# Optimization experiments

Hardware: AMD Instinct MI355X
Metric: run time of the kernel (lower is better)

The kernel has to match this reference:

```python
import jax, jax.numpy as jnp
import numpy as np

N, E = 2048, 262144
H, EH, NH, FF = 96, 64, 12, 192
DH = H // NH
NITERS, NLAYERS = 2, 3


def _leaky(x):
    return jax.nn.leaky_relu(x, 0.01)


def _ln(x, s, b):
    m = x.mean(-1, keepdims=True)
    v = ((x - m) ** 2).mean(-1, keepdims=True)
    return (x - m) / jnp.sqrt(v + 1e-5) * s + b


def _encoder(x, qkv_w, qkv_b, out_w, out_b, l1s, l1b, fw1, fb1, fw2, fb2, l2s, l2b):
    qkv = x @ qkv_w + qkv_b  # [N, 3H]
    q, k, v = jnp.split(qkv, 3, axis=-1)
    q = q.reshape(-1, NH, DH)
    k = k.reshape(-1, NH, DH)
    v = v.reshape(-1, NH, DH)
    att = jax.nn.softmax(jnp.einsum('nhd,mhd->hnm', q, k) / jnp.sqrt(jnp.float32(DH)), axis=-1)
    o = jnp.einsum('hnm,mhd->nhd', att, v).reshape(-1, H) @ out_w + out_b
    x = _ln(x + o, l1s, l1b)
    f = jax.nn.relu(x @ fw1 + fb1) @ fw2 + fb2
    return _ln(x + f, l2s, l2b)


def setup_inputs() -> dict:
    key = jax.random.key(0)
    ks = iter(jax.random.split(key, 64))
    def p(shape, scale=0.05):
        return (jax.random.normal(next(ks), shape) * scale).astype(jnp.float32)
    inp = {}
    inp['X'] = jax.random.normal(next(ks), (N, 19), dtype=jnp.float32)
    inp['edge_features'] = jax.random.uniform(next(ks), (E, 12), dtype=jnp.float32)
    inp['edge_index'] = jax.random.randint(next(ks), (E, 2), 0, N, dtype=jnp.int32)
    inp['node_scaler'] = jnp.ones((19,), jnp.float32)
    inp['edge_scaler'] = jnp.ones((12,), jnp.float32)
    inp['in_w1'] = p((19, H)); inp['in_b1'] = p((H,))
    inp['in_w2'] = p((H, H)); inp['in_b2'] = p((H,))
    inp['enc_qkv_w'] = p((NLAYERS, H, 3 * H)); inp['enc_qkv_b'] = p((NLAYERS, 3 * H))
    inp['enc_out_w'] = p((NLAYERS, H, H)); inp['enc_out_b'] = p((NLAYERS, H))
    inp['enc_ln1_s'] = jnp.ones((NLAYERS, H), jnp.float32); inp['enc_ln1_b'] = jnp.zeros((NLAYERS, H), jnp.float32)
    inp['enc_ff_w1'] = p((NLAYERS, H, FF)); inp['enc_ff_b1'] = p((NLAYERS, FF))
    inp['enc_ff_w2'] = p((NLAYERS, FF, H)); inp['enc_ff_b2'] = p((NLAYERS, H))
    inp['enc_ln2_s'] = jnp.ones((NLAYERS, H), jnp.float32); inp['enc_ln2_b'] = jnp.zeros((NLAYERS, H), jnp.float32)
    inp['ein_w1'] = p((12, EH)); inp['ein_b1'] = p((EH,))
    inp['ein_w2'] = p((EH, EH)); inp['ein_b2'] = p((EH,))
    inp['ad_w1'] = p((EH, EH)); inp['ad_b1'] = p((EH,))
    inp['ad_w2'] = p((EH, 1)); inp['ad_b2'] = p((1,))
    inp['ar_w1'] = p((EH, EH)); inp['ar_b1'] = p((EH,))
    inp['ar_w2'] = p((EH, 1)); inp['ar_b2'] = p((1,))
    inp['gc_w1'] = p((NITERS, 2 * H, 2 * H)); inp['gc_b1'] = p((NITERS, 2 * H))
    inp['gc_w2'] = p((NITERS, 2 * H, H)); inp['gc_b2'] = p((NITERS, H))
    inp['en_w1'] = p((2 * H + 12 + EH, H)); inp['en_b1'] = p((H,))
    inp['en_w2'] = p((H, 1)); inp['en_b2'] = p((1,))
    return inp


def reference(X, edge_features, edge_index, node_scaler, edge_scaler,
              in_w1, in_b1, in_w2, in_b2,
              enc_qkv_w, enc_qkv_b, enc_out_w, enc_out_b,
              enc_ln1_s, enc_ln1_b, enc_ff_w1, enc_ff_b1, enc_ff_w2, enc_ff_b2,
              enc_ln2_s, enc_ln2_b,
              ein_w1, ein_b1, ein_w2, ein_b2,
              ad_w1, ad_b1, ad_w2, ad_b2,
              ar_w1, ar_b1, ar_w2, ar_b2,
              gc_w1, gc_b1, gc_w2, gc_b2,
              en_w1, en_b1, en_w2, en_b2):
    ef = (edge_features + 1e-4) / edge_scaler
    x = X / node_scaler
    # edge feature MLP + direct/reverse attention weights
    ef_nn = _leaky(_leaky(ef @ ein_w1 + ein_b1) @ ein_w2 + ein_b2)
    a_dir = jax.nn.sigmoid(_leaky(ef_nn @ ad_w1 + ad_b1) @ ad_w2 + ad_b2)
    a_rev = jax.nn.sigmoid(_leaky(ef_nn @ ar_w1 + ar_b1) @ ar_w2 + ar_b2)
    alpha = jnp.concatenate([a_dir, a_rev], axis=0)  # [2E, 1]
    # node input MLP + transformer encoder over all N nodes
    h = _leaky(_leaky(x @ in_w1 + in_b1) @ in_w2 + in_b2)
    for i in range(NLAYERS):
        h = _encoder(h, enc_qkv_w[i], enc_qkv_b[i], enc_out_w[i], enc_out_b[i],
                     enc_ln1_s[i], enc_ln1_b[i], enc_ff_w1[i], enc_ff_b1[i],
                     enc_ff_w2[i], enc_ff_b2[i], enc_ln2_s[i], enc_ln2_b[i])
    src = edge_index[:, 0]
    dst = edge_index[:, 1]
    zeros_n = jnp.zeros((N,), edge_index.dtype)
    ind1 = jnp.concatenate([zeros_n, src, dst])  # destinations, [N + 2E]
    ind2 = jnp.concatenate([zeros_n, dst, src])  # sources
    alpha_full = jnp.concatenate([jnp.ones((N, 1), h.dtype), alpha], axis=0)
    for i in range(NITERS):
        m = jnp.concatenate([h[ind1], h[ind2]], axis=-1)  # [N+2E, 2H]
        m = _leaky(_leaky(m @ gc_w1[i] + gc_b1[i]) @ gc_w2[i] + gc_b2[i])
        num = jax.ops.segment_sum(alpha_full * m, ind1, num_segments=N)
        den = jax.ops.segment_sum(alpha_full, ind1, num_segments=N)
        h = num / (den + 1e-8)
    e = jnp.concatenate([h[src], h[dst], ef_nn, ef], axis=-1)
    pred = jax.nn.sigmoid(_leaky(e @ en_w1 + en_b1) @ en_w2 + en_b2)
    return pred
```

## Files before the change

kernel.cpp:

```cpp
#include <hip/hip_runtime.h>

#define NN 2048
#define EE 262144

typedef __attribute__((ext_vector_type(8))) short bf16x8;
typedef __attribute__((ext_vector_type(4))) float f32x4;
typedef unsigned int u32;
typedef unsigned short u16;

__device__ __forceinline__ u16 f2bf(float f){
  u32 u = __builtin_bit_cast(u32, f);
  u32 r = u + 0x7FFFu + ((u >> 16) & 1u);
  return (u16)(r >> 16);
}
__device__ __forceinline__ float bf2f(u16 h){
  u32 u = ((u32)h) << 16;
  return __builtin_bit_cast(float, u);
}
__device__ __forceinline__ int swzb(int byte, int row){ return byte ^ ((row & 7) << 4); }
__device__ __forceinline__ float lrelu(float v){ return v > 0.f ? v : 0.01f * v; }

static const size_t WS_WT    = 0;
static const size_t WS_EFNN  = 772096;
static const size_t WS_ALPHA = WS_EFNN  + 33554432;
static const size_t WS_H     = WS_ALPHA + 2097152;
static const size_t WS_QKV   = WS_H     + 786432;
static const size_t WS_OBUF  = WS_QKV   + 2359296;
static const size_t WS_TMPA  = WS_OBUF  + 786432;
static const size_t WS_TMPB  = WS_TMPA  + 786432;
static const size_t WS_X1    = WS_TMPB  + 1572864;
static const size_t WS_NUM   = WS_X1    + 786432;
static const size_t WS_DEN   = WS_NUM   + 786432;
static const size_t WS_XS    = WS_DEN   + 8192;
static const size_t WS_HBF   = WS_XS    + 155648;
static const size_t WS_SIDX  = WS_HBF   + 393216;
static const size_t WS_ALPS  = WS_SIDX  + 4194304;
static const size_t WS_CNT   = WS_ALPS  + 2097152;
static const size_t WS_OFFS  = WS_CNT   + 8192;
static const size_t WS_PK    = WS_OFFS  + 8192;

#define IN1T 0
#define IN2T 3072
#define QKVT 12288
#define OUTT 95232
#define FF1T 122880
#define FF2T 178176
#define EIN1T 233472
#define EIN2T 235520
#define AD1T 239616
#define AR1T 243712
#define GC1T 247808
#define GC2T 321536
#define ENAT 358400
#define ENBT 367616
#define ENCT 376832
#define POOL_TOT 386048

#define PK_EIN1 0
#define PK_EIN2 2048
#define PK_AD1  6144
#define PK_AR1  10240
#define PK_GC2  14336
#define PK_ENC  51200
#define PK_QKV  60416
#define PK_OUT  143360
#define PK_FF1  171008
#define PK_FF2  226304
#define PK_IN1  281600
#define PK_IN2  284672
#define PK_GC1A 293888
#define PK_GC1B 330752
#define PK_ENA  367616
#define PK_ENB  376832
#define PK_TOT  386048

struct CvtJobs {
  const float* src[27];
  int K[27], Nc[27], Kp[27];
  int cum[28];
};

__global__ __launch_bounds__(256) void k_cvt(CvtJobs jb, u16* __restrict__ pool){
  int i = blockIdx.x * 256 + threadIdx.x;
  if (i >= jb.cum[27]) return;
  int j = 0;
  while (i >= jb.cum[j + 1]) j++;
  int loc = i - jb.cum[j];
  int Kp = jb.Kp[j];
  int n = loc / Kp, k = loc - n * Kp;
  float v = (k < jb.K[j]) ? jb.src[j][(size_t)k * jb.Nc[j] + n] : 0.f;
  pool[i] = f2bf(v);
}

struct PkJobs {
  int srcOff[27], Nc16[27], Kp[27];
  int cum[28];
};

__global__ __launch_bounds__(256) void k_pack(PkJobs jb, const u16* __restrict__ pool,
                                              u16* __restrict__ pk){
  int i = blockIdx.x * 256 + threadIdx.x;
  if (i >= jb.cum[27]) return;
  int j = 0;
  while (i >= jb.cum[j + 1]) j++;
  int loc = i - jb.cum[j];
  int jj = loc & 7, lane = (loc >> 3) & 63, tk = loc >> 9;
// ... 48 lines not shown
  int pos = offs[i1] + r;
  sidx[pos] = make_int2(i1, i2);
  alphaS[pos] = alpha[g];
}

__global__ __launch_bounds__(256) void k_dens(const int* __restrict__ offs, const float* __restrict__ alphaS,
                                              float* __restrict__ den){
  int n = blockIdx.x * 4 + (threadIdx.x >> 6);
  int lane = threadIdx.x & 63;
  int b = offs[n], e = offs[n + 1];
  float s = 0.f;
  for (int i = b + lane; i < e; i += 64) s += alphaS[i];
  #pragma unroll
  for (int st = 1; st < 64; st <<= 1) s += __shfl_xor(s, st);
  if (lane == 0) den[n] = s + (n == 0 ? 2048.f : 0.f);
}

template<int NT, int KS, int SR, int NC16>
__device__ __forceinline__ void tile_gemm_gp(const char* sm, int aBase, const u16* __restrict__ Wp,
                                             int lane, f32x4* acc){
  const int r15 = lane & 15;
  const int kb = (lane >> 4) * 16;
  #pragma unroll
  for (int ks = 0; ks < KS; ks++){
    bf16x8 a = *(const bf16x8*)(sm + aBase + swzb(r15*SR + ks*64 + kb, r15));
    #pragma unroll
    for (int ct = 0; ct < NT; ct++){
      bf16x8 b = *(const bf16x8*)(Wp + (((size_t)ks*NC16 + ct)*64 + lane)*8);
      acc[ct] = __builtin_amdgcn_mfma_f32_16x16x32_bf16(a, b, acc[ct], 0, 0, 0);
    }
  }
}

template<int NT, int KS, int MODE, int ACT>
__global__ __launch_bounds__(256) void k_gemm2(const float* __restrict__ A, int K, int NcTot, int Nc16Tot,
    const u16* __restrict__ pkW, const float* __restrict__ bias, float* __restrict__ C,
    float* __restrict__ C2, const float* __restrict__ R, const float* __restrict__ sc,
    const float* __restrict__ bi)
{
  constexpr int Kpad = KS * 32;
  constexpr int SR = (Kpad*2 + 127) / 128 * 128;
  __shared__ __align__(16) char smem[32*SR + 256];
  const int tid = threadIdx.x;
  const int row0 = blockIdx.x * 32;
  for (int j = tid; j < 32*(Kpad/2); j += 256){
    int r = j / (Kpad/2); int c = (j - r*(Kpad/2)) * 2;
    const float* ap = A + (size_t)(row0 + r)*K + c;
    float f0 = (c < K) ? ap[0] : 0.f;
    float f1 = (c + 1 < K) ? ap[1] : 0.f;
    *(u32*)(smem + swzb(r*SR + c*2, r)) = (u32)f2bf(f0) | ((u32)f2bf(f1) << 16);
  }
  __syncthreads();
  const int lane = tid & 63, w = tid >> 6;
  const int wr = w >> 1, wc = w & 1;
  const int r15 = lane & 15;
  const int kb = (lane >> 4) * 16;
  f32x4 acc[NT] = {};
  #pragma unroll
  for (int ks = 0; ks < KS; ks++){
    int row = wr*16 + r15;
    bf16x8 a = *(const bf16x8*)(smem + swzb(row*SR + ks*64 + kb, row));
    #pragma unroll
    for (int ct = 0; ct < NT; ct++){
      int t16g = blockIdx.y*(2*NT) + wc*NT + ct;
      bf16x8 b = *(const bf16x8*)(pkW + (((size_t)ks*Nc16Tot + t16g)*64 + lane)*8);
      acc[ct] = __builtin_amdgcn_mfma_f32_16x16x32_bf16(a, b, acc[ct], 0, 0, 0);
    }
  }
  const int colbase = blockIdx.y*(NT*32) + wc*(NT*16);
  if (MODE != 2){
    #pragma unroll
    for (int ct = 0; ct < NT; ct++){
      int col = colbase + ct*16 + r15;
      float bs = bias ? bias[col] : 0.f;
      #pragma unroll
      for (int q = 0; q < 4; q++){
        int row = row0 + wr*16 + (lane >> 4)*4 + q;
        float v = acc[ct][q] + bs;
        if (ACT == 1) v = lrelu(v);
        if (ACT == 2) v = v > 0.f ? v : 0.f;
        if (MODE == 0){
          C[(size_t)row*NcTot + col] = v;
// ... 186 lines not shown
  for (int j = tid; j < 2048; j += 256){
    int r = j >> 5;
    ((u32*)efnn)[e0*32 + j] = *(const u32*)(smem + swzb(r*128 + (j&31)*4, r));
  }
  { f32x4 acc[4] = {};
    tile_gemm_gp<4,2,128,4>(smem, w*2048, pk + PK_AD1, lane, acc);
    store_lds(acc, 8192, adb1); }
  __syncthreads();
  { int row = tid >> 2, part = tid & 3;
    float s = 0.f;
    #pragma unroll
    for (int i = 0; i < 16; i++){
      int k = part*16 + i;
      s += bf2f(*(const u16*)(smem + 8192 + swzb(row*128 + k*2, row))) * adw2[k];
    }
    s += __shfl_xor(s, 1); s += __shfl_xor(s, 2);
    if (part == 0) alpha[e0 + row] = 1.f / (1.f + __expf(-(s + adb2[0]))); }
  __syncthreads();
  { f32x4 acc[4] = {};
    tile_gemm_gp<4,2,128,4>(smem, w*2048, pk + PK_AR1, lane, acc);
    store_lds(acc, 8192, arb1); }
  __syncthreads();
  { int row = tid >> 2, part = tid & 3;
    float s = 0.f;
    #pragma unroll
    for (int i = 0; i < 16; i++){
      int k = part*16 + i;
      s += bf2f(*(const u16*)(smem + 8192 + swzb(row*128 + k*2, row))) * arw2[k];
    }
    s += __shfl_xor(s, 1); s += __shfl_xor(s, 2);
    if (part == 0) alpha[EE + e0 + row] = 1.f / (1.f + __expf(-(s + arb2[0]))); }
}

__global__ __launch_bounds__(256) void k_gc5x(const float* __restrict__ P1, const float* __restrict__ P2,
    const int2* __restrict__ sidx, const float* __restrict__ alphaS, const int* __restrict__ offs,
    const u16* __restrict__ wt2p, const float* __restrict__ b2, const float* __restrict__ den,
    float* __restrict__ hout)
{
  __shared__ __align__(16) char smem[26624];
  float* p1c  = (float*)(smem + 24576);
  int*   i2b  = (int*)  (smem + 25344);
  float* alph = (float*)(smem + 25600);
  float* part = (float*)(smem + 25856);
  const int tid = threadIdx.x;
  const int lane = tid & 63, w = tid >> 6;
  const int wr = w >> 1, wc = w & 1;
  const int r15 = lane & 15;
  const int kb = (lane >> 4) * 16;
  const int n = blockIdx.x;
  const int rbeg = offs[n], rend = offs[n + 1];
  if (tid < 48) ((float4*)p1c)[tid] = ((const float4*)(P1 + (size_t)n*192))[tid];
  bf16x8 Bf[6][3];
  #pragma unroll
  for (int ks = 0; ks < 6; ks++)
    #pragma unroll
    for (int ct = 0; ct < 3; ct++)
      Bf[ks][ct] = *(const bf16x8*)(wt2p + (((size_t)ks*6 + wc*3 + ct)*64 + lane)*8);
  float b2r[3];
  #pragma unroll
  for (int ct = 0; ct < 3; ct++) b2r[ct] = b2[wc*48 + ct*16 + r15];
  float cs0 = 0.f, cs1 = 0.f, cs2 = 0.f;

  const int total = rend - rbeg + (n == 0 ? 1 : 0);
  const int nch = (total + 63) >> 6;
  for (int c = 0; c < nch; c++){
    int base = rbeg + c*64;
    if (tid < 64){
      int pos = base + tid;
      if (pos < rend){ i2b[tid] = sidx[pos].y; alph[tid] = alphaS[pos]; }
      else if (n == 0 && pos == rend){ i2b[tid] = 0; alph[tid] = 2048.f; }
      else { i2b[tid] = 0; alph[tid] = 0.f; }
    }
    __syncthreads();
    for (int j = tid; j < 1536; j += 256){
      int r = j / 24, q = j - (j/24)*24;
      int c8 = q * 8;
      const float* p2 = P2 + (size_t)i2b[r]*192 + c8;
      float4 b0 = *(const float4*)p2, b1 = *(const float4*)(p2 + 4);
      const float* pc = p1c + c8;
      u16 pkv[8];
      pkv[0]=f2bf(lrelu(pc[0]+b0.x)); pkv[1]=f2bf(lrelu(pc[1]+b0.y));
      pkv[2]=f2bf(lrelu(pc[2]+b0.z)); pkv[3]=f2bf(lrelu(pc[3]+b0.w));
      pkv[4]=f2bf(lrelu(pc[4]+b1.x)); pkv[5]=f2bf(lrelu(pc[5]+b1.y));
      pkv[6]=f2bf(lrelu(pc[6]+b1.z)); pkv[7]=f2bf(lrelu(pc[7]+b1.w));
      *(bf16x8*)(smem + swzb(r*384 + c8*2, r)) = *(bf16x8*)pkv;
    }
    __syncthreads();
    float ar[2][4];
    #pragma unroll
    for (int rt = 0; rt < 2; rt++)
      #pragma unroll
      for (int q = 0; q < 4; q++)
        ar[rt][q] = alph[wr*32 + rt*16 + (lane >> 4)*4 + q];
    f32x4 acc2[2][3] = {};
    #pragma unroll
    for (int ks = 0; ks < 6; ks++){
      bf16x8 a[2];
      #pragma unroll
      for (int rt = 0; rt < 2; rt++){
        int row = wr*32 + rt*16 + r15;
        a[rt] = *(const bf16x8*)(smem + swzb(row*384 + ks*64 + kb, row));
      }
      #pragma unroll
      for (int ct = 0; ct < 3; ct++)
        #pragma unroll
        for (int rt = 0; rt < 2; rt++)
          acc2[rt][ct] = __builtin_amdgcn_mfma_f32_16x16x32_bf16(a[rt], Bf[ks][ct], acc2[rt][ct], 0, 0, 0);
    }
    #pragma unroll
    for (int rt = 0; rt < 2; rt++){
      #pragma unroll
      for (int q = 0; q < 4; q++){
        float aw = ar[rt][q];
        cs0 += aw * lrelu(acc2[rt][0][q] + b2r[0]);
        cs1 += aw * lrelu(acc2[rt][1][q] + b2r[1]);
        cs2 += aw * lrelu(acc2[rt][2][q] + b2r[2]);
      }
    }
    __syncthreads();
  }
  #pragma unroll
  for (int stx = 16; stx < 64; stx <<= 1){
    cs0 += __shfl_xor(cs0, stx);
    cs1 += __shfl_xor(cs1, stx);
    cs2 += __shfl_xor(cs2, stx);
  }
  if (lane < 16){
    part[(w*3 + 0)*16 + lane] = cs0;
    part[(w*3 + 1)*16 + lane] = cs1;
    part[(w*3 + 2)*16 + lane] = cs2;
  }
  __syncthreads();
  if (tid < 96){
    int wc2 = tid / 48, rem = tid - wc2*48;
    int ct = rem / 16, rr = rem - ct*16;
    float tot = part[(wc2*3 + ct)*16 + rr] + part[((2 + wc2)*3 + ct)*16 + rr];
    hout[(size_t)n*96 + tid] = tot / (den[n] + 1e-8f);
  }
}

__global__ __launch_bounds__(256) void k_final2(const float* __restrict__ hp1, const float* __restrict__ hp2,
    const int* __restrict__ ei, const u16* __restrict__ efnn, const float* __restrict__ efr,
    const float* __restrict__ es, const u16* __restrict__ encp,
    const float* __restrict__ enw2, const float* __restrict__ enb2, float* __restrict__ out)
{
  __shared__ __align__(16) char smem[38144];
  float* etb = (float*)(smem + 12288);
  float* w2s = (float*)(smem + 37120);
  int*   eix = (int*)  (smem + 37504);
  const int tid = threadIdx.x;
  const int e0 = blockIdx.x * 64;
  for (int j = tid; j < 768; j += 256){
    int r = j / 12, q = j - (j/12)*12;
    int e = e0 + r;
    bf16x8 v;
    if (q < 8){
      v = *(const bf16x8*)(efnn + (size_t)e*64 + q*8);
    } else if (q < 10){
      u16 pkv[8];
      #pragma unroll
      for (int i = 0; i < 8; i++){
        int cc = (q - 8)*8 + i;
        pkv[i] = (cc < 12) ? f2bf((efr[(size_t)e*12 + cc] + 1e-4f) / es[cc]) : (u16)0;
      }
      v = *(bf16x8*)pkv;
    } else {
      v = bf16x8{0,0,0,0,0,0,0,0};
    }
    *(bf16x8*)(smem + swzb(r*192 + q*16, r)) = v;
  }
  if (tid < 96) w2s[tid] = enw2[tid];
  if (tid < 64){ eix[2*tid] = ei[2*(e0+tid)]; eix[2*tid+1] = ei[2*(e0+tid)+1]; }
  __syncthreads();
  const int lane = tid & 63, w = tid >> 6;
  const int r15 = lane & 15;
  f32x4 acc[6] = {};
  tile_gemm_gp<6,3,192,6>(smem, w*16*192, encp, lane, acc);
  #pragma unroll
  for (int ct = 0; ct < 6; ct++){
    int col = ct*16 + r15;
    #pragma unroll
    for (int q = 0; q < 4; q++){
      int row = w*16 + (lane >> 4)*4 + q;
      etb[row*97 + col] = acc[ct][q];
    }
  }
  __syncthreads();
  int r = tid >> 2, part = tid & 3;
  int s1 = eix[2*r], s2 = eix[2*r + 1];
  const float* p1 = hp1 + (size_t)s1*96 + part*24;
  const float* p2 = hp2 + (size_t)s2*96 + part*24;
  const float* et = etb + r*97 + part*24;
  const float* wz = w2s + part*24;
  float s = 0.f;
  #pragma unroll
  for (int i = 0; i < 24; i++){
    float v = et[i] + p1[i] + p2[i];
    s += lrelu(v) * wz[i];
  }
  s += __shfl_xor(s, 1); s += __shfl_xor(s, 2);
  if (part == 0) out[e0 + r] = 1.f / (1.f + __expf(-(s + enb2[0])));
}

extern "C" void kernel_launch(void* const* d_in, const int* in_sizes, int n_in,
                              void* d_out, int out_size, void* d_ws, size_t ws_size,
                              hipStream_t stream) {
  (void)in_sizes; (void)n_in; (void)out_size; (void)ws_size;
  const float* X      = (const float*)d_in[0];
  const float* EFR    = (const float*)d_in[1];
  const int*   EI     = (const int*)  d_in[2];
  const float* NS     = (const float*)d_in[3];
  const float* ES     = (const float*)d_in[4];
  const float* IN_W1  = (const float*)d_in[5];
  const float* IN_B1  = (const float*)d_in[6];
  const float* IN_W2  = (const float*)d_in[7];
  const float* IN_B2  = (const float*)d_in[8];
  const float* QKV_W  = (const float*)d_in[9];
  const float* QKV_B  = (const float*)d_in[10];
  const float* OUT_W  = (const float*)d_in[11];
  const float* OUT_B  = (const float*)d_in[12];
  const float* LN1S   = (const float*)d_in[13];
  const float* LN1B   = (const float*)d_in[14];
  const float* FFW1   = (const float*)d_in[15];
  const float* FFB1   = (const float*)d_in[16];
  const float* FFW2   = (const float*)d_in[17];
  const float* FFB2   = (const float*)d_in[18];
  const float* LN2S   = (const float*)d_in[19];
  const float* LN2B   = (const float*)d_in[20];
  const float* EIN_W1 = (const float*)d_in[21];
  const float* EIN_B1 = (const float*)d_in[22];
  const float* EIN_W2 = (const float*)d_in[23];
  const float* EIN_B2 = (const float*)d_in[24];
  const float* AD_W1  = (const float*)d_in[25];
  const float* AD_B1  = (const float*)d_in[26];
  const float* AD_W2  = (const float*)d_in[27];
  const float* AD_B2  = (const float*)d_in[28];
  const float* AR_W1  = (const float*)d_in[29];
  const float* AR_B1  = (const float*)d_in[30];
  const float* AR_W2  = (const float*)d_in[31];
  const float* AR_B2  = (const float*)d_in[32];
  const float* GC_W1  = (const float*)d_in[33];
  const float* GC_B1  = (const float*)d_in[34];
  const float* GC_W2  = (const float*)d_in[35];
  const float* GC_B2  = (const float*)d_in[36];
  const float* EN_W1  = (const float*)d_in[37];
  const float* EN_B1  = (const float*)d_in[38];
  const float* EN_W2  = (const float*)d_in[39];
  const float* EN_B2  = (const float*)d_in[40];

  char* ws = (char*)d_ws;
  u16*   pool   = (u16*)  (ws + WS_WT);
  u16*   efnn   = (u16*)  (ws + WS_EFNN);
  float* alpha  = (float*)(ws + WS_ALPHA);
  float* h      = (float*)(ws + WS_H);
  float* qkvb   = (float*)(ws + WS_QKV);
  float* obuf   = (float*)(ws + WS_OBUF);
  float* tmpA   = (float*)(ws + WS_TMPA);
  float* tmpB   = (float*)(ws + WS_TMPB);
  float* x1     = (float*)(ws + WS_X1);
  float* den    = (float*)(ws + WS_DEN);
  float* xs     = (float*)(ws + WS_XS);
  int2*  sidx   = (int2*) (ws + WS_SIDX);
  float* alphaS = (float*)(ws + WS_ALPS);
  int*   cnt    = (int*)  (ws + WS_CNT);
  int*   offs   = (int*)  (ws + WS_OFFS);
  u16*   pk     = (u16*)  (ws + WS_PK);
  float* P1     = (float*)(ws + WS_QKV);
  float* P2     = (float*)(ws + WS_TMPB);
  float* hp1    = (float*)(ws + WS_OBUF);
  float* hp2    = (float*)(ws + WS_TMPA);
  float* kvp    = (float*)(ws + WS_ALPHA);

  CvtJobs jb;
  int idx = 0, cum = 0;
  auto addjob = [&](const float* s, int K, int Nc, int Kp){
    jb.src[idx] = s; jb.K[idx] = K; jb.Nc[idx] = Nc; jb.Kp[idx] = Kp;
    jb.cum[idx] = cum; cum += Nc * Kp; idx++;
  };
  addjob(IN_W1, 19, 96, 32);
  addjob(IN_W2, 96, 96, 96);
  for (int l = 0; l < 3; l++) addjob(QKV_W + (size_t)l*96*288, 96, 288, 96);
  for (int l = 0; l < 3; l++) addjob(OUT_W + (size_t)l*96*96,  96, 96,  96);
  for (int l = 0; l < 3; l++) addjob(FFW1  + (size_t)l*96*192, 96, 192, 96);
  for (int l = 0; l < 3; l++) addjob(FFW2  + (size_t)l*192*96, 192, 96, 192);
  addjob(EIN_W1, 12, 64, 32);
  addjob(EIN_W2, 64, 64, 64);
  addjob(AD_W1,  64, 64, 64);
  addjob(AR_W1,  64, 64, 64);
  for (int i = 0; i < 2; i++){
    addjob(GC_W1 + (size_t)i*192*192,          96, 192, 96);
    addjob(GC_W1 + (size_t)i*192*192 + 96*192, 96, 192, 96);
  }
  for (int i = 0; i < 2; i++) addjob(GC_W2 + (size_t)i*192*96, 192, 96, 192);
  addjob(EN_W1,            96, 96, 96);
  addjob(EN_W1 + 96*96,    96, 96, 96);
  addjob(EN_W1 + 192*96,   76, 96, 96);
  jb.cum[idx] = cum;

  k_cvt<<<(POOL_TOT + 255)/256, 256, 0, stream>>>(jb, pool);

  PkJobs pj;
  int pidx = 0, pcum = 0;
  auto addpk = [&](int srcOff, int Nc16, int Ks, int Kp){
    pj.srcOff[pidx] = srcOff; pj.Nc16[pidx] = Nc16; pj.Kp[pidx] = Kp;
    pj.cum[pidx] = pcum; pcum += Nc16 * Ks * 512; pidx++;
  };
  addpk(EIN1T, 4, 1, 32);
  addpk(EIN2T, 4, 2, 64);
  addpk(AD1T,  4, 2, 64);
  addpk(AR1T,  4, 2, 64);
  addpk(GC2T,          6, 6, 192);
  addpk(GC2T + 18432,  6, 6, 192);
  addpk(ENCT, 6, 3, 96);
  for (int l = 0; l < 3; l++) addpk(QKVT + l*27648, 18, 3, 96);
  for (int l = 0; l < 3; l++) addpk(OUTT + l*9216,   6, 3, 96);
  for (int l = 0; l < 3; l++) addpk(FF1T + l*18432, 12, 3, 96);
  for (int l = 0; l < 3; l++) addpk(FF2T + l*18432,  6, 6, 192);
  addpk(IN1T, 6, 1, 32);
  addpk(IN2T, 6, 3, 96);
  for (int i = 0; i < 2; i++) addpk(GC1T + i*36864,         12, 3, 96);
  for (int i = 0; i < 2; i++) addpk(GC1T + i*36864 + 18432, 12, 3, 96);
  addpk(ENAT, 6, 3, 96);
  addpk(ENBT, 6, 3, 96);
  pj.cum[pidx] = pcum;

  k_pack<<<(PK_TOT + 255)/256, 256, 0, stream>>>(pj, pool, pk);

  k_xscale<<<(NN*19 + 255)/256, 256, 0, stream>>>(X, NS, xs);
  k_gemm2<3,1,0,1><<<dim3(64,1), 256, 0, stream>>>(xs, 19, 96, 6, pk + PK_IN1, IN_B1, tmpA,
                                                   nullptr, nullptr, nullptr, nullptr);
  k_gemm2<3,3,0,1><<<dim3(64,1), 256, 0, stream>>>(tmpA, 96, 96, 6, pk + PK_IN2, IN_B2, h,
                                                   nullptr, nullptr, nullptr, nullptr);

  k_edge<<<EE/64, 256, 0, stream>>>(EFR, ES, pk, EIN_B1, EIN_B2,
                                    AD_B1, AD_W2, AD_B2, AR_B1, AR_W2, AR_B2, efnn, alpha);

  (void)hipMemsetAsync(cnt, 0, NN*4, stream);
  k_hist<<<(2*EE)/256, 256, 0, stream>>>(EI, cnt);
  k_scan<<<1, 256, 0, stream>>>(cnt, offs);
  (void)hipMemsetAsync(cnt, 0, NN*4, stream);
  k_scatter<<<(2*EE)/256, 256, 0, stream>>>(EI, alpha, offs, cnt, sidx, alphaS);
  k_dens<<<NN/4, 256, 0, stream>>>(offs, alphaS, den);

  for (int l = 0; l < 3; l++){
    k_gemm2<3,3,1,0><<<dim3(64,3), 256, 0, stream>>>(h, 96, 288, 18, pk + PK_QKV + l*27648,
                                                     QKV_B + l*288, qkvb, kvp, nullptr, nullptr, nullptr);
    k_attn5<<<1536, 256, 0, stream>>>(qkvb, kvp, obuf);
    k_gemm2<3,3,2,0><<<dim3(64,1), 256, 0, stream>>>(obuf, 96, 96, 6, pk + PK_OUT + l*9216,
                                                     OUT_B + l*96, x1, nullptr, h, LN1S + l*96, LN1B + l*96);
    k_gemm2<3,3,0,2><<<dim3(64,2), 256, 0, stream>>>(x1, 96, 192, 12, pk + PK_FF1 + l*18432,
                                                     FFB1 + l*192, tmpB, nullptr, nullptr, nullptr, nullptr);
    k_gemm2<3,6,2,0><<<dim3(64,1), 256, 0, stream>>>(tmpB, 192, 96, 6, pk + PK_FF2 + l*18432,
                                                     FFB2 + l*96, h, nullptr, x1, LN2S + l*96, LN2B + l*96);
  }

  for (int it = 0; it < 2; it++){
    k_gemm2<3,3,0,0><<<dim3(64,2), 256, 0, stream>>>(h, 96, 192, 12, pk + PK_GC1A + it*18432,
                                                     nullptr, P1, nullptr, nullptr, nullptr, nullptr);
    k_gemm2<3,3,0,0><<<dim3(64,2), 256, 0, stream>>>(h, 96, 192, 12, pk + PK_GC1B + it*18432,
                                                     GC_B1 + it*192, P2, nullptr, nullptr, nullptr, nullptr);
    k_gc5x<<<NN, 256, 0, stream>>>(P1, P2, sidx, alphaS, offs,
                                   pk + PK_GC2 + it*18432, GC_B2 + it*96, den, h);
  }

  k_gemm2<3,3,0,0><<<dim3(64,1), 256, 0, stream>>>(h, 96, 96, 6, pk + PK_ENA, nullptr, hp1,
                                                   nullptr, nullptr, nullptr, nullptr);
  k_gemm2<3,3,0,0><<<dim3(64,1), 256, 0, stream>>>(h, 96, 96, 6, pk + PK_ENB, EN_B1, hp2,
                                                   nullptr, nullptr, nullptr, nullptr);
  k_final2<<<EE/64, 256, 0, stream>>>(hp1, hp2, EI, efnn, EFR, ES,
                                      pk + PK_ENC, EN_W2, EN_B2, (float*)d_out);
}
```

Measured before the change: 598.5 us.

## Build GC message MFMA operands directly in registers, dropping LDS staging

The graph-conv aggregation kernel now gathers P2 rows and forms the bf16 A-fragments directly in registers per lane, feeding MFMA without writing to and reading back from shared memory. This removes the per-chunk LDS tile and two of the three block barriers per chunk. Alpha weights are broadcast via shuffles, and launch bounds request two blocks per SM. The cost is more redundant or less coalesced global loads per lane and higher register pressure. Leaky ReLU is also rewritten as fmax.

Result: slower. 701.1 us (+17.1%).

```diff
diff --git a/kernel.cpp b/kernel.cpp
--- a/kernel.cpp
+++ b/kernel.cpp
@@ -18,7 +18,7 @@
   return __builtin_bit_cast(float, u);
 }
 __device__ __forceinline__ int swzb(int byte, int row){ return byte ^ ((row & 7) << 4); }
-__device__ __forceinline__ float lrelu(float v){ return v > 0.f ? v : 0.01f * v; }
+__device__ __forceinline__ float lrelu(float v){ return fmaxf(v, 0.01f * v); }
 
 static const size_t WS_WT    = 0;
 static const size_t WS_EFNN  = 772096;
@@ -454,21 +454,18 @@
     if (part == 0) alpha[EE + e0 + row] = 1.f / (1.f + __expf(-(s + arb2[0]))); }
 }
 
-__global__ __launch_bounds__(256) void k_gc5x(const float* __restrict__ P1, const float* __restrict__ P2,
+__global__ __launch_bounds__(256, 2) void k_gc6(const float* __restrict__ P1, const float* __restrict__ P2,
     const int2* __restrict__ sidx, const float* __restrict__ alphaS, const int* __restrict__ offs,
     const u16* __restrict__ wt2p, const float* __restrict__ b2, const float* __restrict__ den,
     float* __restrict__ hout)
 {
-  __shared__ __align__(16) char smem[26624];
-  float* p1c  = (float*)(smem + 24576);
-  int*   i2b  = (int*)  (smem + 25344);
-  float* alph = (float*)(smem + 25600);
-  float* part = (float*)(smem + 25856);
+  __shared__ __align__(16) float p1c[192];
+  __shared__ float part[12][16];
   const int tid = threadIdx.x;
   const int lane = tid & 63, w = tid >> 6;
   const int wr = w >> 1, wc = w & 1;
   const int r15 = lane & 15;
-  const int kb = (lane >> 4) * 16;
+  const int q16 = lane >> 4;
   const int n = blockIdx.x;
   const int rbeg = offs[n], rend = offs[n + 1];
   if (tid < 48) ((float4*)p1c)[tid] = ((const float4*)(P1 + (size_t)n*192))[tid];
@@ -481,65 +478,54 @@
   float b2r[3];
   #pragma unroll
   for (int ct = 0; ct < 3; ct++) b2r[ct] = b2[wc*48 + ct*16 + r15];
+  __syncthreads();
   float cs0 = 0.f, cs1 = 0.f, cs2 = 0.f;
 
   const int total = rend - rbeg + (n == 0 ? 1 : 0);
   const int nch = (total + 63) >> 6;
   for (int c = 0; c < nch; c++){
-    int base = rbeg + c*64;
-    if (tid < 64){
-      int pos = base + tid;
-      if (pos < rend){ i2b[tid] = sidx[pos].y; alph[tid] = alphaS[pos]; }
-      else if (n == 0 && pos == rend){ i2b[tid] = 0; alph[tid] = 2048.f; }
-      else { i2b[tid] = 0; alph[tid] = 0.f; }
-    }
-    __syncthreads();
-    for (int j = tid; j < 1536; j += 256){
-      int r = j / 24, q = j - (j/24)*24;
-      int c8 = q * 8;
-      const float* p2 = P2 + (size_t)i2b[r]*192 + c8;
-      float4 b0 = *(const float4*)p2, b1 = *(const float4*)(p2 + 4);
-      const float* pc = p1c + c8;
-      u16 pkv[8];
-      pkv[0]=f2bf(lrelu(pc[0]+b0.x)); pkv[1]=f2bf(lrelu(pc[1]+b0.y));
-      pkv[2]=f2bf(lrelu(pc[2]+b0.z)); pkv[3]=f2bf(lrelu(pc[3]+b0.w));
-      pkv[4]=f2bf(lrelu(pc[4]+b1.x)); pkv[5]=f2bf(lrelu(pc[5]+b1.y));
-      pkv[6]=f2bf(lrelu(pc[6]+b1.z)); pkv[7]=f2bf(lrelu(pc[7]+b1.w));
-      *(bf16x8*)(smem + swzb(r*384 + c8*2, r)) = *(bf16x8*)pkv;
-    }
-    __syncthreads();
-    float ar[2][4];
-    #pragma unroll
-    for (int rt = 0; rt < 2; rt++)
-      #pragma unroll
-      for (int q = 0; q < 4; q++)
-        ar[rt][q] = alph[wr*32 + rt*16 + (lane >> 4)*4 + q];
     f32x4 acc2[2][3] = {};
-    #pragma unroll
-    for (int ks = 0; ks < 6; ks++){
-      bf16x8 a[2];
-      #pragma unroll
-      for (int rt = 0; rt < 2; rt++){
-        int row = wr*32 + rt*16 + r15;
-        a[rt] = *(const bf16x8*)(smem + swzb(row*384 + ks*64 + kb, row));
-      }
-      #pragma unroll
-      for (int ct = 0; ct < 3; ct++)
-        #pragma unroll
-        for (int rt = 0; rt < 2; rt++)
-          acc2[rt][ct] = __builtin_amdgcn_mfma_f32_16x16x32_bf16(a[rt], Bf[ks][ct], acc2[rt][ct], 0, 0, 0);
-    }
+    float alr[2];
     #pragma unroll
     for (int rt = 0; rt < 2; rt++){
+      int pos = rbeg + c*64 + wr*32 + rt*16 + r15;
+      int i2 = 0; float al = 0.f;
+      if (pos < rend){ int2 sx = sidx[pos]; i2 = sx.y; al = alphaS[pos]; }
+      else if (n == 0 && pos == rend){ al = 2048.f; }
+      alr[rt] = al;
+      const float* p2r = P2 + (size_t)i2*192 + q16*8;
+      const float* p1r = p1c + q16*8;
+      #pragma unroll
+      for (int ks = 0; ks < 6; ks++){
+        float4 a0 = *(const float4*)(p2r + ks*32);
+        float4 a1 = *(const float4*)(p2r + ks*32 + 4);
+        float4 p0 = *(const float4*)(p1r + ks*32);
+        float4 p1v = *(const float4*)(p1r + ks*32 + 4);
+        u16 pkv[8];
+        pkv[0] = f2bf(lrelu(p0.x + a0.x));
+        pkv[1] = f2bf(lrelu(p0.y + a0.y));
+        pkv[2] = f2bf(lrelu(p0.z + a0.z));
+        pkv[3] = f2bf(lrelu(p0.w + a0.w));
+        pkv[4] = f2bf(lrelu(p1v.x + a1.x));
+        pkv[5] = f2bf(lrelu(p1v.y + a1.y));
+        pkv[6] = f2bf(lrelu(p1v.z + a1.z));
+        pkv[7] = f2bf(lrelu(p1v.w + a1.w));
+        bf16x8 af = *(bf16x8*)pkv;
+        acc2[rt][0] = __builtin_amdgcn_mfma_f32_16x16x32_bf16(af, Bf[ks][0], acc2[rt][0], 0, 0, 0);
+        acc2[rt][1] = __builtin_amdgcn_mfma_f32_16x16x32_bf16(af, Bf[ks][1], acc2[rt][1], 0, 0, 0);
+        acc2[rt][2] = __builtin_amdgcn_mfma_f32_16x16x32_bf16(af, Bf[ks][2], acc2[rt][2], 0, 0, 0);
+      }
+    }
+    #pragma unroll
+    for (int rt = 0; rt < 2; rt++){
       #pragma unroll
       for (int q = 0; q < 4; q++){
-        float aw = ar[rt][q];
+        float aw = __shfl(alr[rt], (lane & 48) | (q16*4 + q));
         cs0 += aw * lrelu(acc2[rt][0][q] + b2r[0]);
         cs1 += aw * lrelu(acc2[rt][1][q] + b2r[1]);
         cs2 += aw * lrelu(acc2[rt][2][q] + b2r[2]);
       }
     }
-    __syncthreads();
   }
   #pragma unroll
   for (int stx = 16; stx < 64; stx <<= 1){
@@ -548,15 +534,15 @@
     cs2 += __shfl_xor(cs2, stx);
   }
   if (lane < 16){
-    part[(w*3 + 0)*16 + lane] = cs0;
-    part[(w*3 + 1)*16 + lane] = cs1;
-    part[(w*3 + 2)*16 + lane] = cs2;
+    part[w*3 + 0][lane] = cs0;
+    part[w*3 + 1][lane] = cs1;
+    part[w*3 + 2][lane] = cs2;
   }
   __syncthreads();
   if (tid < 96){
     int wc2 = tid / 48, rem = tid - wc2*48;
     int ct = rem / 16, rr = rem - ct*16;
-    float tot = part[(wc2*3 + ct)*16 + rr] + part[((2 + wc2)*3 + ct)*16 + rr];
+    float tot = part[wc2*3 + ct][rr] + part[(2 + wc2)*3 + ct][rr];
     hout[(size_t)n*96 + tid] = tot / (den[n] + 1e-8f);
   }
 }
@@ -781,8 +767,8 @@
                                                      nullptr, P1, nullptr, nullptr, nullptr, nullptr);
     k_gemm2<3,3,0,0><<<dim3(64,2), 256, 0, stream>>>(h, 96, 192, 12, pk + PK_GC1B + it*18432,
                                                      GC_B1 + it*192, P2, nullptr, nullptr, nullptr, nullptr);
-    k_gc5x<<<NN, 256, 0, stream>>>(P1, P2, sidx, alphaS, offs,
-                                   pk + PK_GC2 + it*18432, GC_B2 + it*96, den, h);
+    k_gc6<<<NN, 256, 0, stream>>>(P1, P2, sidx, alphaS, offs,
+                                  pk + PK_GC2 + it*18432, GC_B2 + it*96, den, h);
   }
 
   k_gemm2<3,3,0,0><<<dim3(64,1), 256, 0, stream>>>(h, 96, 96, 6, pk + PK_ENA, nullptr, hp1,
```

## Double-buffer gather in graph-conv kernel with register prefetch of next chunk

Applied to the files above, without the earlier changes.

Rewrites the per-node graph-conv aggregation kernel to prefetch the next 64-edge chunk's P2 rows into registers while the MFMA on the current chunk runs. It uses two LDS buffers so one barrier per chunk suffices. B-weight fragments are now loaded from global inside the MFMA loop instead of being held in registers, and alpha is read directly from global in the epilogue, removing the shared index/alpha staging. This trades register pressure from the prefetch buffers against more global/L1 traffic for weights, and doubles LDS use, which may lower occupancy.

Result: slower. 629.0 us (+5.1%).

```diff
diff --git a/kernel.cpp b/kernel.cpp
--- a/kernel.cpp
+++ b/kernel.cpp
@@ -18,7 +18,7 @@
   return __builtin_bit_cast(float, u);
 }
 __device__ __forceinline__ int swzb(int byte, int row){ return byte ^ ((row & 7) << 4); }
-__device__ __forceinline__ float lrelu(float v){ return v > 0.f ? v : 0.01f * v; }
+__device__ __forceinline__ float lrelu(float v){ return fmaxf(v, 0.01f * v); }
 
 static const size_t WS_WT    = 0;
 static const size_t WS_EFNN  = 772096;
@@ -454,16 +454,14 @@
     if (part == 0) alpha[EE + e0 + row] = 1.f / (1.f + __expf(-(s + arb2[0]))); }
 }
 
-__global__ __launch_bounds__(256) void k_gc5x(const float* __restrict__ P1, const float* __restrict__ P2,
+__global__ __launch_bounds__(256) void k_gc7(const float* __restrict__ P1, const float* __restrict__ P2,
     const int2* __restrict__ sidx, const float* __restrict__ alphaS, const int* __restrict__ offs,
     const u16* __restrict__ wt2p, const float* __restrict__ b2, const float* __restrict__ den,
     float* __restrict__ hout)
 {
-  __shared__ __align__(16) char smem[26624];
-  float* p1c  = (float*)(smem + 24576);
-  int*   i2b  = (int*)  (smem + 25344);
-  float* alph = (float*)(smem + 25600);
-  float* part = (float*)(smem + 25856);
+  __shared__ __align__(16) char smem[50688];
+  float* p1c  = (float*)(smem + 49152);
+  float* part = (float*)(smem + 49920);
   const int tid = threadIdx.x;
   const int lane = tid & 63, w = tid >> 6;
   const int wr = w >> 1, wc = w & 1;
@@ -472,48 +470,52 @@
   const int n = blockIdx.x;
   const int rbeg = offs[n], rend = offs[n + 1];
   if (tid < 48) ((float4*)p1c)[tid] = ((const float4*)(P1 + (size_t)n*192))[tid];
-  bf16x8 Bf[6][3];
-  #pragma unroll
-  for (int ks = 0; ks < 6; ks++)
-    #pragma unroll
-    for (int ct = 0; ct < 3; ct++)
-      Bf[ks][ct] = *(const bf16x8*)(wt2p + (((size_t)ks*6 + wc*3 + ct)*64 + lane)*8);
   float b2r[3];
   #pragma unroll
   for (int ct = 0; ct < 3; ct++) b2r[ct] = b2[wc*48 + ct*16 + r15];
-  float cs0 = 0.f, cs1 = 0.f, cs2 = 0.f;
+  __syncthreads();
 
   const int total = rend - rbeg + (n == 0 ? 1 : 0);
   const int nch = (total + 63) >> 6;
+
+  float4 va[6], vb[6];
+  auto load_chunk = [&](int c){
+    #pragma unroll
+    for (int s = 0; s < 6; s++){
+      int j = tid + s*256;
+      int r = j / 24, q = j - (j/24)*24;
+      int pos = rbeg + c*64 + r;
+      int i2 = (pos < rend) ? sidx[pos].y : 0;
+      const float* p2r = P2 + (size_t)i2*192 + q*8;
+      va[s] = *(const float4*)p2r;
+      vb[s] = *(const float4*)(p2r + 4);
+    }
+  };
+  load_chunk(0);
+  float cs0 = 0.f, cs1 = 0.f, cs2 = 0.f;
+
   for (int c = 0; c < nch; c++){
-    int base = rbeg + c*64;
-    if (tid < 64){
-      int pos = base + tid;
-      if (pos < rend){ i2b[tid] = sidx[pos].y; alph[tid] = alphaS[pos]; }
-      else if (n == 0 && pos == rend){ i2b[tid] = 0; alph[tid] = 2048.f; }
-      else { i2b[tid] = 0; alph[tid] = 0.f; }
-    }
-    __syncthreads();
-    for (int j = tid; j < 1536; j += 256){
+    char* ab = smem + (c & 1)*24576;
+    #pragma unroll
+    for (int s = 0; s < 6; s++){
+      int j = tid + s*256;
       int r = j / 24, q = j - (j/24)*24;
-      int c8 = q * 8;
-      const float* p2 = P2 + (size_t)i2b[r]*192 + c8;
-      float4 b0 = *(const float4*)p2, b1 = *(const float4*)(p2 + 4);
+      int c8 = q*8;
       const float* pc = p1c + c8;
       u16 pkv[8];
-      pkv[0]=f2bf(lrelu(pc[0]+b0.x)); pkv[1]=f2bf(lrelu(pc[1]+b0.y));
-      pkv[2]=f2bf(lrelu(pc[2]+b0.z)); pkv[3]=f2bf(lrelu(pc[3]+b0.w));
-      pkv[4]=f2bf(lrelu(pc[4]+b1.x)); pkv[5]=f2bf(lrelu(pc[5]+b1.y));
-      pkv[6]=f2bf(lrelu(pc[6]+b1.z)); pkv[7]=f2bf(lrelu(pc[7]+b1.w));
-      *(bf16x8*)(smem + swzb(r*384 + c8*2, r)) = *(bf16x8*)pkv;
+      pkv[0] = f2bf(lrelu(pc[0] + va[s].x));
+      pkv[1] = f2bf(lrelu(pc[1] + va[s].y));
+      pkv[2] = f2bf(lrelu(pc[2] + va[s].z));
+      pkv[3] = f2bf(lrelu(pc[3] + va[s].w));
+      pkv[4] = f2bf(lrelu(pc[4] + vb[s].x));
+      pkv[5] = f2bf(lrelu(pc[5] + vb[s].y));
+      pkv[6] = f2bf(lrelu(pc[6] + vb[s].z));
+      pkv[7] = f2bf(lrelu(pc[7] + vb[s].w));
+      *(bf16x8*)(ab + swzb(r*384 + c8*2, r)) = *(bf16x8*)pkv;
     }
     __syncthreads();
-    float ar[2][4];
-    #pragma unroll
-    for (int rt = 0; rt < 2; rt++)
-      #pragma unroll
-      for (int q = 0; q < 4; q++)
-        ar[rt][q] = alph[wr*32 + rt*16 + (lane >> 4)*4 + q];
+    if (c + 1 < nch) load_chunk(c + 1);
+
     f32x4 acc2[2][3] = {};
     #pragma unroll
     for (int ks = 0; ks < 6; ks++){
@@ -521,25 +523,28 @@
       #pragma unroll
       for (int rt = 0; rt < 2; rt++){
         int row = wr*32 + rt*16 + r15;
-        a[rt] = *(const bf16x8*)(smem + swzb(row*384 + ks*64 + kb, row));
-      }
-      #pragma unroll
-      for (int ct = 0; ct < 3; ct++)
+        a[rt] = *(const bf16x8*)(ab + swzb(row*384 + ks*64 + kb, row));
+      }
+      #pragma unroll
+      for (int ct = 0; ct < 3; ct++){
+        bf16x8 b = *(const bf16x8*)(wt2p + (((size_t)ks*6 + wc*3 + ct)*64 + lane)*8);
         #pragma unroll
         for (int rt = 0; rt < 2; rt++)
-          acc2[rt][ct] = __builtin_amdgcn_mfma_f32_16x16x32_bf16(a[rt], Bf[ks][ct], acc2[rt][ct], 0, 0, 0);
+          acc2[rt][ct] = __builtin_amdgcn_mfma_f32_16x16x32_bf16(a[rt], b, acc2[rt][ct], 0, 0, 0);
+      }
     }
     #pragma unroll
     for (int rt = 0; rt < 2; rt++){
       #pragma unroll
       for (int q = 0; q < 4; q++){
-        float aw = ar[rt][q];
+        int row = wr*32 + rt*16 + (lane >> 4)*4 + q;
+        int pos = rbeg + c*64 + row;
+        float aw = (pos < rend) ? alphaS[pos] : ((n == 0 && pos == rend) ? 2048.f : 0.f);
         cs0 += aw * lrelu(acc2[rt][0][q] + b2r[0]);
         cs1 += aw * lrelu(acc2[rt][1][q] + b2r[1]);
         cs2 += aw * lrelu(acc2[rt][2][q] + b2r[2]);
       }
     }
-    __syncthreads();
   }
   #pragma unroll
   for (int stx = 16; stx < 64; stx <<= 1){
@@ -781,8 +786,8 @@
                                                      nullptr, P1, nullptr, nullptr, nullptr, nullptr);
     k_gemm2<3,3,0,0><<<dim3(64,2), 256, 0, stream>>>(h, 96, 192, 12, pk + PK_GC1B + it*18432,
                                                      GC_B1 + it*192, P2, nullptr, nullptr, nullptr, nullptr);
-    k_gc5x<<<NN, 256, 0, stream>>>(P1, P2, sidx, alphaS, offs,
-                                   pk + PK_GC2 + it*18432, GC_B2 + it*96, den, h);
+    k_gc7<<<NN, 256, 0, stream>>>(P1, P2, sidx, alphaS, offs,
+                                  pk + PK_GC2 + it*18432, GC_B2 + it*96, den, h);
   }
 
   k_gemm2<3,3,0,0><<<dim3(64,1), 256, 0, stream>>>(h, 96, 96, 6, pk + PK_ENA, nullptr, hp1,
```

## Split graph-conv node blocks across two CTAs and fuse paired projection GEMMs

Applied to the files above, without the earlier changes.

The per-node graph-conv kernel now runs two blocks per node, each taking alternate 64-edge chunks, and combines partial sums with atomicAdd into a num buffer. The normalization by den moves into the following GEMM's A-load. The two GC1 projections and the two final-stage projections are each merged into one wider GEMM launch. The weight fragments of the second layer are now loaded per k-step instead of being held in registers. This aims to cut launch count, improve load balance and occupancy on skewed node degrees, and reduce register pressure, at the cost of atomics, an extra memset, and more global weight loads.

Measured after the change: 597.5 us. No clear change (-0.2%).

```diff
diff --git a/kernel.cpp b/kernel.cpp
--- a/kernel.cpp
+++ b/kernel.cpp
@@ -18,7 +18,7 @@
   return __builtin_bit_cast(float, u);
 }
 __device__ __forceinline__ int swzb(int byte, int row){ return byte ^ ((row & 7) << 4); }
-__device__ __forceinline__ float lrelu(float v){ return v > 0.f ? v : 0.01f * v; }
+__device__ __forceinline__ float lrelu(float v){ return fmaxf(v, 0.01f * v); }
 
 static const size_t WS_WT    = 0;
 static const size_t WS_EFNN  = 772096;
@@ -68,10 +68,8 @@
 #define PK_FF2  226304
 #define PK_IN1  281600
 #define PK_IN2  284672
-#define PK_GC1A 293888
-#define PK_GC1B 330752
-#define PK_ENA  367616
-#define PK_ENB  376832
+#define PK_GC1  293888
+#define PK_ENAB 367616
 #define PK_TOT  386048
 
 struct CvtJobs {
@@ -186,11 +184,11 @@
   }
 }
 
-template<int NT, int KS, int MODE, int ACT>
+template<int NT, int KS, int MODE, int ACT, int DIVA = 0>
 __global__ __launch_bounds__(256) void k_gemm2(const float* __restrict__ A, int K, int NcTot, int Nc16Tot,
     const u16* __restrict__ pkW, const float* __restrict__ bias, float* __restrict__ C,
     float* __restrict__ C2, const float* __restrict__ R, const float* __restrict__ sc,
-    const float* __restrict__ bi)
+    const float* __restrict__ bi, const float* __restrict__ dden)
 {
   constexpr int Kpad = KS * 32;
   constexpr int SR = (Kpad*2 + 127) / 128 * 128;
@@ -202,6 +200,10 @@
     const float* ap = A + (size_t)(row0 + r)*K + c;
     float f0 = (c < K) ? ap[0] : 0.f;
     float f1 = (c + 1 < K) ? ap[1] : 0.f;
+    if (DIVA){
+      float dv = 1.f / (dden[row0 + r] + 1e-8f);
+      f0 *= dv; f1 *= dv;
+    }
     *(u32*)(smem + swzb(r*SR + c*2, r)) = (u32)f2bf(f0) | ((u32)f2bf(f1) << 16);
   }
   __syncthreads();
@@ -454,10 +456,10 @@
     if (part == 0) alpha[EE + e0 + row] = 1.f / (1.f + __expf(-(s + arb2[0]))); }
 }
 
-__global__ __launch_bounds__(256) void k_gc5x(const float* __restrict__ P1, const float* __restrict__ P2,
+__global__ __launch_bounds__(256) void k_gc8(const float* __restrict__ P,
     const int2* __restrict__ sidx, const float* __restrict__ alphaS, const int* __restrict__ offs,
-    const u16* __restrict__ wt2p, const float* __restrict__ b2, const float* __restrict__ den,
-    float* __restrict__ hout)
+    const u16* __restrict__ wt2p, const float* __restrict__ b1, const float* __restrict__ b2,
+    float* __restrict__ num)
 {
   __shared__ __align__(16) char smem[26624];
   float* p1c  = (float*)(smem + 24576);
@@ -469,15 +471,9 @@
   const int wr = w >> 1, wc = w & 1;
   const int r15 = lane & 15;
   const int kb = (lane >> 4) * 16;
-  const int n = blockIdx.x;
+  const int n = blockIdx.x >> 1, sp = blockIdx.x & 1;
   const int rbeg = offs[n], rend = offs[n + 1];
-  if (tid < 48) ((float4*)p1c)[tid] = ((const float4*)(P1 + (size_t)n*192))[tid];
-  bf16x8 Bf[6][3];
-  #pragma unroll
-  for (int ks = 0; ks < 6; ks++)
-    #pragma unroll
-    for (int ct = 0; ct < 3; ct++)
-      Bf[ks][ct] = *(const bf16x8*)(wt2p + (((size_t)ks*6 + wc*3 + ct)*64 + lane)*8);
+  if (tid < 192) p1c[tid] = P[(size_t)n*384 + tid] + b1[tid];
   float b2r[3];
   #pragma unroll
   for (int ct = 0; ct < 3; ct++) b2r[ct] = b2[wc*48 + ct*16 + r15];
@@ -485,7 +481,8 @@
 
   const int total = rend - rbeg + (n == 0 ? 1 : 0);
   const int nch = (total + 63) >> 6;
-  for (int c = 0; c < nch; c++){
+  __syncthreads();
+  for (int c = sp; c < nch; c += 2){
     int base = rbeg + c*64;
     if (tid < 64){
       int pos = base + tid;
@@ -497,14 +494,14 @@
     for (int j = tid; j < 1536; j += 256){
       int r = j / 24, q = j - (j/24)*24;
       int c8 = q * 8;
-      const float* p2 = P2 + (size_t)i2b[r]*192 + c8;
-      float4 b0 = *(const float4*)p2, b1 = *(const float4*)(p2 + 4);
+      const float* p2 = P + (size_t)i2b[r]*384 + 192 + c8;
+      float4 b0 = *(const float4*)p2, b1v = *(const float4*)(p2 + 4);
       const float* pc = p1c + c8;
       u16 pkv[8];
       pkv[0]=f2bf(lrelu(pc[0]+b0.x)); pkv[1]=f2bf(lrelu(pc[1]+b0.y));
       pkv[2]=f2bf(lrelu(pc[2]+b0.z)); pkv[3]=f2bf(lrelu(pc[3]+b0.w));
-      pkv[4]=f2bf(lrelu(pc[4]+b1.x)); pkv[5]=f2bf(lrelu(pc[5]+b1.y));
-      pkv[6]=f2bf(lrelu(pc[6]+b1.z)); pkv[7]=f2bf(lrelu(pc[7]+b1.w));
+      pkv[4]=f2bf(lrelu(pc[4]+b1v.x)); pkv[5]=f2bf(lrelu(pc[5]+b1v.y));
+      pkv[6]=f2bf(lrelu(pc[6]+b1v.z)); pkv[7]=f2bf(lrelu(pc[7]+b1v.w));
       *(bf16x8*)(smem + swzb(r*384 + c8*2, r)) = *(bf16x8*)pkv;
     }
     __syncthreads();
@@ -524,10 +521,12 @@
         a[rt] = *(const bf16x8*)(smem + swzb(row*384 + ks*64 + kb, row));
       }
       #pragma unroll
-      for (int ct = 0; ct < 3; ct++)
+      for (int ct = 0; ct < 3; ct++){
+        bf16x8 b = *(const bf16x8*)(wt2p + (((size_t)ks*6 + wc*3 + ct)*64 + lane)*8);
         #pragma unroll
         for (int rt = 0; rt < 2; rt++)
-          acc2[rt][ct] = __builtin_amdgcn_mfma_f32_16x16x32_bf16(a[rt], Bf[ks][ct], acc2[rt][ct], 0, 0, 0);
+          acc2[rt][ct] = __builtin_amdgcn_mfma_f32_16x16x32_bf16(a[rt], b, acc2[rt][ct], 0, 0, 0);
+      }
     }
     #pragma unroll
     for (int rt = 0; rt < 2; rt++){
@@ -557,19 +556,20 @@
     int wc2 = tid / 48, rem = tid - wc2*48;
     int ct = rem / 16, rr = rem - ct*16;
     float tot = part[(wc2*3 + ct)*16 + rr] + part[((2 + wc2)*3 + ct)*16 + rr];
-    hout[(size_t)n*96 + tid] = tot / (den[n] + 1e-8f);
-  }
-}
-
-__global__ __launch_bounds__(256) void k_final2(const float* __restrict__ hp1, const float* __restrict__ hp2,
+    atomicAdd(num + (size_t)n*96 + tid, tot);
+  }
+}
+
+__global__ __launch_bounds__(256) void k_final3(const float* __restrict__ hp,
     const int* __restrict__ ei, const u16* __restrict__ efnn, const float* __restrict__ efr,
-    const float* __restrict__ es, const u16* __restrict__ encp,
+    const float* __restrict__ es, const u16* __restrict__ encp, const float* __restrict__ enb1,
     const float* __restrict__ enw2, const float* __restrict__ enb2, float* __restrict__ out)
 {
-  __shared__ __align__(16) char smem[38144];
+  __shared__ __align__(16) char smem[38400];
   float* etb = (float*)(smem + 12288);
   float* w2s = (float*)(smem + 37120);
-  int*   eix = (int*)  (smem + 37504);
+  float* b1s = (float*)(smem + 37504);
+  int*   eix = (int*)  (smem + 37888);
   const int tid = threadIdx.x;
   const int e0 = blockIdx.x * 64;
   for (int j = tid; j < 768; j += 256){
@@ -592,6 +592,7 @@
     *(bf16x8*)(smem + swzb(r*192 + q*16, r)) = v;
   }
   if (tid < 96) w2s[tid] = enw2[tid];
+  else if (tid < 192) b1s[tid - 96] = enb1[tid - 96];
   if (tid < 64){ eix[2*tid] = ei[2*(e0+tid)]; eix[2*tid+1] = ei[2*(e0+tid)+1]; }
   __syncthreads();
   const int lane = tid & 63, w = tid >> 6;
@@ -610,14 +611,15 @@
   __syncthreads();
   int r = tid >> 2, part = tid & 3;
   int s1 = eix[2*r], s2 = eix[2*r + 1];
-  const float* p1 = hp1 + (size_t)s1*96 + part*24;
-  const float* p2 = hp2 + (size_t)s2*96 + part*24;
+  const float* p1 = hp + (size_t)s1*192 + part*24;
+  const float* p2 = hp + (size_t)s2*192 + 96 + part*24;
   const float* et = etb + r*97 + part*24;
   const float* wz = w2s + part*24;
+  const float* bz = b1s + part*24;
   float s = 0.f;
   #pragma unroll
   for (int i = 0; i < 24; i++){
-    float v = et[i] + p1[i] + p2[i];
+    float v = et[i] + p1[i] + p2[i] + bz[i];
     s += lrelu(v) * wz[i];
   }
   s += __shfl_xor(s, 1); s += __shfl_xor(s, 2);
@@ -680,6 +682,7 @@
   float* tmpA   = (float*)(ws + WS_TMPA);
   float* tmpB   = (float*)(ws + WS_TMPB);
   float* x1     = (float*)(ws + WS_X1);
+  float* num    = (float*)(ws + WS_NUM);
   float* den    = (float*)(ws + WS_DEN);
   float* xs     = (float*)(ws + WS_XS);
   int2*  sidx   = (int2*) (ws + WS_SIDX);
@@ -687,10 +690,8 @@
   int*   cnt    = (int*)  (ws + WS_CNT);
   int*   offs   = (int*)  (ws + WS_OFFS);
   u16*   pk     = (u16*)  (ws + WS_PK);
-  float* P1     = (float*)(ws + WS_QKV);
-  float* P2     = (float*)(ws + WS_TMPB);
-  float* hp1    = (float*)(ws + WS_OBUF);
-  float* hp2    = (float*)(ws + WS_TMPA);
+  float* P      = (float*)(ws + WS_QKV);
+  float* hp     = (float*)(ws + WS_TMPB);
   float* kvp    = (float*)(ws + WS_ALPHA);
 
   CvtJobs jb;
@@ -740,19 +741,17 @@
   for (int l = 0; l < 3; l++) addpk(FF2T + l*18432,  6, 6, 192);
   addpk(IN1T, 6, 1, 32);
   addpk(IN2T, 6, 3, 96);
-  for (int i = 0; i < 2; i++) addpk(GC1T + i*36864,         12, 3, 96);
-  for (int i = 0; i < 2; i++) addpk(GC1T + i*36864 + 18432, 12, 3, 96);
-  addpk(ENAT, 6, 3, 96);
-  addpk(ENBT, 6, 3, 96);
-  pj.cum[pidx] = pcum;
+  for (int i = 0; i < 2; i++) addpk(GC1T + i*36864, 24, 3, 96);
+  addpk(ENAT, 12, 3, 96);
+  for (int z = pidx; z <= 27; z++) pj.cum[z] = pcum;
 
   k_pack<<<(PK_TOT + 255)/256, 256, 0, stream>>>(pj, pool, pk);
 
   k_xscale<<<(NN*19 + 255)/256, 256, 0, stream>>>(X, NS, xs);
   k_gemm2<3,1,0,1><<<dim3(64,1), 256, 0, stream>>>(xs, 19, 96, 6, pk + PK_IN1, IN_B1, tmpA,
-                                                   nullptr, nullptr, nullptr, nullptr);
+                                                   nullptr, nullptr, nullptr, nullptr, nullptr);
   k_gemm2<3,3,0,1><<<dim3(64,1), 256, 0, stream>>>(tmpA, 96, 96, 6, pk + PK_IN2, IN_B2, h,
-                                                   nullptr, nullptr, nullptr, nullptr);
+                                                   nullptr, nullptr, nullptr, nullptr, nullptr);
 
   k_edge<<<EE/64, 256, 0, stream>>>(EFR, ES, pk, EIN_B1, EIN_B2,
                                     AD_B1, AD_W2, AD_B2, AR_B1, AR_W2, AR_B2, efnn, alpha);
@@ -766,29 +765,31 @@
 
   for (int l = 0; l < 3; l++){
     k_gemm2<3,3,1,0><<<dim3(64,3), 256, 0, stream>>>(h, 96, 288, 18, pk + PK_QKV + l*27648,
-                                                     QKV_B + l*288, qkvb, kvp, nullptr, nullptr, nullptr);
+                                                     QKV_B + l*288, qkvb, kvp, nullptr, nullptr, nullptr, nullptr);
     k_attn5<<<1536, 256, 0, stream>>>(qkvb, kvp, obuf);
     k_gemm2<3,3,2,0><<<dim3(64,1), 256, 0, stream>>>(obuf, 96, 96, 6, pk + PK_OUT + l*9216,
-                                                     OUT_B + l*96, x1, nullptr, h, LN1S + l*96, LN1B + l*96);
+                                                     OUT_B + l*96, x1, nullptr, h, LN1S + l*96, LN1B + l*96, nullptr);
     k_gemm2<3,3,0,2><<<dim3(64,2), 256, 0, stream>>>(x1, 96, 192, 12, pk + PK_FF1 + l*18432,
-                                                     FFB1 + l*192, tmpB, nullptr, nullptr, nullptr, nullptr);
+                                                     FFB1 + l*192, tmpB, nullptr, nullptr, nullptr, nullptr, nullptr);
     k_gemm2<3,6,2,0><<<dim3(64,1), 256, 0, stream>>>(tmpB, 192, 96, 6, pk + PK_FF2 + l*18432,
-                                                     FFB2 + l*96, h, nullptr, x1, LN2S + l*96, LN2B + l*96);
+                                                     FFB2 + l*96, h, nullptr, x1, LN2S + l*96, LN2B + l*96, nullptr);
   }
 
   for (int it = 0; it < 2; it++){
-    k_gemm2<3,3,0,0><<<dim3(64,2), 256, 0, stream>>>(h, 96, 192, 12, pk + PK_GC1A + it*18432,
-                                                     nullptr, P1, nullptr, nullptr, nullptr, nullptr);
-    k_gemm2<3,3,0,0><<<dim3(64,2), 256, 0, stream>>>(h, 96, 192, 12, pk + PK_GC1B + it*18432,
-                                                     GC_B1 + it*192, P2, nullptr, nullptr, nullptr, nullptr);
-    k_gc5x<<<NN, 256, 0, stream>>>(P1, P2, sidx, alphaS, offs,
-                                   pk + PK_GC2 + it*18432, GC_B2 + it*96, den, h);
-  }
-
-  k_gemm2<3,3,0,0><<<dim3(64,1), 256, 0, stream>>>(h, 96, 96, 6, pk + PK_ENA, nullptr, hp1,
-                                                   nullptr, nullptr, nullptr, nullptr);
-  k_gemm2<3,3,0,0><<<dim3(64,1), 256, 0, stream>>>(h, 96, 96, 6, pk + PK_ENB, EN_B1, hp2,
-                                                   nullptr, nullptr, nullptr, nullptr);
-  k_final2<<<EE/64, 256, 0, stream>>>(hp1, hp2, EI, efnn, EFR, ES,
-                                      pk + PK_ENC, EN_W2, EN_B2, (float*)d_out);
-}
+    if (it == 0){
+      k_gemm2<3,3,0,0><<<dim3(64,3), 256, 0, stream>>>(h, 96, 384, 24, pk + PK_GC1 + it*36864,
+                                                       nullptr, P, nullptr, nullptr, nullptr, nullptr, nullptr);
+    } else {
+      k_gemm2<3,3,0,0,1><<<dim3(64,3), 256, 0, stream>>>(num, 96, 384, 24, pk + PK_GC1 + it*36864,
+                                                         nullptr, P, nullptr, nullptr, nullptr, nullptr, den);
+    }
+    (void)hipMemsetAsync(num, 0, NN*96*4, stream);
+    k_gc8<<<2*NN, 256, 0, stream>>>(P, sidx, alphaS, offs,
+                                    pk + PK_GC2 + it*18432, GC_B1 + it*192, GC_B2 + it*96, num);
+  }
+
+  k_gemm2<3,3,0,0,1><<<dim3(64,2), 256, 0, stream>>>(num, 96, 192, 12, pk + PK_ENAB,
+                                                     nullptr, hp, nullptr, nullptr, nullptr, nullptr, den);
+  k_final3<<<EE/64, 256, 0, stream>>>(hp, EI, efnn, EFR, ES,
+                                      pk + PK_ENC, EN_B1, EN_W2, EN_B2, (float*)d_out);
+}
```
